# Kernel optimization log

Measured on AMD Instinct MI355X. Metric: run time of the kernel, lower is better.

## Reference

```python
import jax, jax.numpy as jnp
import numpy as np

BN_EPS = 1e-5


def setup_inputs() -> dict:
    key = jax.random.key(0)
    ks = jax.random.split(key, 6)
    B, C, N, K, T, O = 8, 64, 4096, 20, 3, 64
    feat = jax.random.normal(ks[0], (B, C, N), dtype=jnp.float32)
    idx = jax.random.randint(ks[1], (B, N, K), 0, N, dtype=jnp.int32)
    group_pc = jax.random.normal(ks[2], (B, 3, N, K), dtype=jnp.float32)
    weights = jax.random.normal(ks[3], (B, 20, T, N, K), dtype=jnp.float32) * 0.05
    conv_w = jax.random.normal(ks[4], (O, C * T, K), dtype=jnp.float32) * 0.02
    gamma = jnp.ones((O,), dtype=jnp.float32)
    beta = jnp.zeros((O,), dtype=jnp.float32)
    return {"feat": feat, "idx": idx, "group_pc": group_pc, "weights": weights,
            "conv_w": conv_w, "gamma": gamma, "beta": beta}


def _poly_terms(group_pc):
    # group_pc: (B, 3, N, K) -> 20 Taylor terms (B, 20, N, K)
    X, Y, Z = group_pc[:, 0], group_pc[:, 1], group_pc[:, 2]
    XX, YY, ZZ = X * X, Y * Y, Z * Z
    XY, XZ, YZ = X * Y, X * Z, Y * Z
    ones = jnp.ones_like(X)
    return jnp.stack([
        ones, X, Y, Z,
        XX, YY, ZZ,
        XX * X, YY * Y, ZZ * Z,
        XY, XZ, YZ,
        X * XY, X * XZ, Y * YZ, Y * XY, Z * XZ, Z * YZ, XY * Z,
    ], axis=1)


def reference(feat, idx, group_pc, weights, conv_w, gamma, beta):
    B, C, N = feat.shape
    K = idx.shape[-1]
    T = weights.shape[2]
    # KNN gather: group_feat[b, c, n, j] = feat[b, c, idx[b, n, j]]  -> (B, C, N, K)
    group_feat = jax.vmap(lambda f, i: f[:, i])(feat, idx)
    # 20 polynomial basis terms of XYZ: (B, 20, N, K)
    terms = _poly_terms(group_pc)
    # taylor[b, t, n, k] = sum_p weights[b, p, t, n, k] * terms[b, p, n, k]
    taylor = jnp.einsum('bptnk,bpnk->btnk', weights, terms)
    # Fused outer-product + [1, K] conv (output width 1, no bias since bn=True):
    # out[b, o, n] = sum_{c, t, k} group_feat[b,c,n,k] * taylor[b,t,n,k] * W[o, c*T+t, k]
    w = conv_w.reshape(conv_w.shape[0], C, T, K)
    out = jnp.einsum('bcnk,btnk,octk->bon', group_feat, taylor, w)
    # BatchNorm (training-mode batch stats over B and N) + ReLU
    mean = jnp.mean(out, axis=(0, 2), keepdims=True)
    var = jnp.var(out, axis=(0, 2), keepdims=True)
    out = gamma[None, :, None] * (out - mean) / jnp.sqrt(var + BN_EPS) + beta[None, :, None]
    return jax.nn.relu(out)
```

## Files before the change

### kernel.cpp

```cpp
#include <hip/hip_runtime.h>
#include <hip/hip_bf16.h>

#define B_ 8
#define C_ 64
#define N_ 4096
#define K_ 20
#define T_ 3
#define O_ 64
#define P_ 20
#define NK_ (N_ * K_)
#define BN_EPS 1e-5f
#define PADW 68

#define WS_FEATT 0
#define WS_WT (WS_FEATT + B_ * N_ * C_)
#define WS_RAW (WS_WT + 122880)
#define WS_PART (WS_RAW + B_ * O_ * N_)
#define WS_STATS (WS_PART + 512 * O_ * 2)

typedef __attribute__((ext_vector_type(8))) _Float16 half8;
typedef __attribute__((ext_vector_type(2))) _Float16 half2v;
typedef __attribute__((ext_vector_type(2))) __fp16 fp16x2;
typedef __attribute__((ext_vector_type(16))) float f32x16;

union UH8 {
    uint4 u;
    half8 h;
    half2v h2[4];
};
union UH2 {
    unsigned u;
    half2v h;
    fp16x2 f;
};

__device__ inline half2v cvt_pkrtz(float a, float b) {
    UH2 x;
    x.f = __builtin_amdgcn_cvt_pkrtz(a, b);
    return x.h;
}
__device__ inline unsigned cvt_pkrtz_u(float a, float b) {
    UH2 x;
    x.f = __builtin_amdgcn_cvt_pkrtz(a, b);
    return x.u;
}

__global__ void k_transpose_feat(const float* __restrict__ feat, float* __restrict__ featT) {
    __shared__ float t[64][65];
    int bid = blockIdx.x;
    int b = bid & 7;
    int n0 = (bid >> 3) << 6;
    int lx = threadIdx.x & 63, ly = threadIdx.x >> 6;
    const float* fp = feat + b * C_ * N_;
#pragma unroll
    for (int cc = 0; cc < 16; ++cc) {
        int c = ly * 16 + cc;
        t[c][lx] = fp[c * N_ + n0 + lx];
    }
    __syncthreads();
    float* op = featT + (b * N_ + n0) * C_;
#pragma unroll
    for (int u = 0; u < 16; ++u) {
        int n = ly * 16 + u;
        op[n * C_ + lx] = t[lx][n];
    }
}

__global__ void k_pack_w(const float* __restrict__ cw, _Float16* __restrict__ Wh) {
    int e = blockIdx.x * 256 + threadIdx.x;
    int j = e & 7;
    int l = (e >> 3) & 63;
    int frag = e >> 9;
    int oh = frag & 1;
    int cc = (frag >> 1) & 3;
    int kt = frag >> 3;
    int t = kt % 3, k = kt / 3;
    int o = oh * 32 + (l & 31);
    int c = cc * 16 + (l >> 5) * 8 + j;
    Wh[e] = (_Float16)cw[o * (C_ * T_ * K_) + (c * T_ + t) * K_ + k];
}

__global__ __launch_bounds__(512, 4) void k_main(const float* __restrict__ featT,
                                                 const _Float16* __restrict__ Wh,
                                                 const float* __restrict__ weights,
                                                 const float* __restrict__ gpc,
                                                 const int* __restrict__ idx,
                                                 float* __restrict__ raw,
                                                 float* __restrict__ part) {
    __shared__ float G[2][64][PADW];
    __shared__ union {
        struct {
            unsigned tayH[3][K_][64];
            int idxS[K_][64];
        } s;
        float out[64][68];
    } su;

    const int bid0 = blockIdx.x;
    const int bid = (bid0 & 7) * 64 + (bid0 >> 3);
    const int b = bid >> 6;
    const int n0 = (bid & 63) << 6;
    const int tid = threadIdx.x;
    const int lane = tid & 63;
    const int wv = tid >> 6;
    const int wc = wv & 3;
    const int wo = wv >> 2;
    const int nl = lane & 31;
    const int kf = lane >> 5;

    {
        const int* ip = idx + (b * N_ + n0) * K_;
        for (int e = tid; e < 64 * K_; e += 512) su.s.idxS[e % K_][e / K_] = ip[e];
    }
    {
        const float* gpcb = gpc + (size_t)b * 3 * NK_ + n0 * K_;
        const float* wb = weights + (size_t)b * P_ * T_ * NK_ + n0 * K_;
        for (int e = tid; e < 64 * K_; e += 512) {
            float X = gpcb[e];
            float Y = gpcb[NK_ + e];
            float Z = gpcb[2 * NK_ + e];
            float XX = X * X, YY = Y * Y, ZZ = Z * Z;
            float XY = X * Y, XZ = X * Z, YZ = Y * Z;
            float terms[20];
            terms[0] = 1.f; terms[1] = X;      terms[2] = Y;       terms[3] = Z;
            terms[4] = XX;  terms[5] = YY;     terms[6] = ZZ;
            terms[7] = XX * X; terms[8] = YY * Y; terms[9] = ZZ * Z;
            terms[10] = XY; terms[11] = XZ;    terms[12] = YZ;
            terms[13] = X * XY;
            terms[14] = X * XZ;
            terms[15] = Y * YZ;
            terms[16] = Y * XY;
            terms[17] = Z * XZ;
            terms[18] = Z * YZ;
            terms[19] = XY * Z;
            float a0 = 0.f, a1 = 0.f, a2 = 0.f;
            const float* wp = wb + e;
#pragma unroll
            for (int p = 0; p < P_; ++p) {
                float tp = terms[p];
                a0 += wp[0] * tp;
                a1 += wp[NK_] * tp;
                a2 += wp[2 * NK_] * tp;
                wp += 3 * NK_;
            }
            int n = e / K_, k = e - n * K_;
            su.s.tayH[0][k][n] = cvt_pkrtz_u(a0, a0);
            su.s.tayH[1][k][n] = cvt_pkrtz_u(a1, a1);
            su.s.tayH[2][k][n] = cvt_pkrtz_u(a2, a2);
        }
    }
    __syncthreads();

    f32x16 acc[2];
#pragma unroll
    for (int nh = 0; nh < 2; ++nh)
#pragma unroll
        for (int i = 0; i < 16; ++i) acc[nh][i] = 0.f;

    const float* fb = featT + (size_t)b * N_ * C_;
    const int r1 = tid >> 4, r2 = r1 + 32, sseg = tid & 15;

    float4 st1 = *(const float4*)(fb + su.s.idxS[0][r1] * C_ + sseg * 4);
    float4 st2 = *(const float4*)(fb + su.s.idxS[0][r2] * C_ + sseg * 4);

    for (int k = 0; k < K_; ++k) {
        float* Gb = &G[k & 1][0][0];
        *(float4*)(Gb + r1 * PADW + sseg * 4) = st1;
        *(float4*)(Gb + r2 * PADW + sseg * 4) = st2;
        __syncthreads();
        if (k + 1 < K_) {
            st1 = *(const float4*)(fb + su.s.idxS[k + 1][r1] * C_ + sseg * 4);
            st2 = *(const float4*)(fb + su.s.idxS[k + 1][r2] * C_ + sseg * 4);
        }
        const float* row0 = Gb + nl * PADW + wc * 16 + kf * 8;
        const float* row1 = Gb + (nl + 32) * PADW + wc * 16 + kf * 8;
        float4 u0 = *(const float4*)row0, u1 = *(const float4*)(row0 + 4);
        float4 w0 = *(const float4*)row1, w1 = *(const float4*)(row1 + 4);
        half2v h0[4], h1[4];
        h0[0] = cvt_pkrtz(u0.x, u0.y);
        h0[1] = cvt_pkrtz(u0.z, u0.w);
        h0[2] = cvt_pkrtz(u1.x, u1.y);
        h0[3] = cvt_pkrtz(u1.z, u1.w);
        h1[0] = cvt_pkrtz(w0.x, w0.y);
        h1[1] = cvt_pkrtz(w0.z, w0.w);
        h1[2] = cvt_pkrtz(w1.x, w1.y);
        h1[3] = cvt_pkrtz(w1.z, w1.w);
#pragma unroll
        for (int t = 0; t < 3; ++t) {
            UH8 ar;
            ar.u = *(const uint4*)(Wh +
                                   (size_t)((((k * 3 + t) * 4 + wc) * 2 + wo) * 64 + lane) * 8);
            UH2 tv0, tv1;
            tv0.u = su.s.tayH[t][k][nl];
            tv1.u = su.s.tayH[t][k][nl + 32];
            UH8 b0, b1;
#pragma unroll
            for (int i = 0; i < 4; ++i) {
                b0.h2[i] = h0[i] * tv0.h;
                b1.h2[i] = h1[i] * tv1.h;
            }
            acc[0] = __builtin_amdgcn_mfma_f32_32x32x16_f16(ar.h, b0.h, acc[0], 0, 0, 0);
            acc[1] = __builtin_amdgcn_mfma_f32_32x32x16_f16(ar.h, b1.h, acc[1], 0, 0, 0);
        }
    }

    __syncthreads();
#pragma unroll 1
    for (int ww = 0; ww < 4; ++ww) {
        if (wc == ww) {
#pragma unroll
            for (int nh = 0; nh < 2; ++nh)
#pragma unroll
                for (int r = 0; r < 16; ++r) {
                    int row = wo * 32 + (r & 3) + ((r >> 2) << 3) + (kf << 2);
                    int col = nh * 32 + nl;
                    if (ww == 0)
                        su.out[row][col] = acc[nh][r];
                    else
                        su.out[row][col] += acc[nh][r];
                }
        }
        __syncthreads();
    }

    if (tid < 256) {
        int o = tid >> 2, seg = tid & 3;
        float4* dst = (float4*)(raw + ((b * O_ + o) * N_) + n0 + seg * 16);
        const float* srow = &su.out[o][seg * 16];
        dst[0] = *(const float4*)&srow[0];
        dst[1] = *(const float4*)&srow[4];
        dst[2] = *(const float4*)&srow[8];
        dst[3] = *(const float4*)&srow[12];
    }
    if (tid < 64) {
        float s1 = 0.f, s2 = 0.f;
#pragma unroll 8
        for (int n = 0; n < 64; ++n) {
            float v = su.out[tid][n];
            s1 += v;
            s2 += v * v;
        }
        part[(bid * 64 + tid) * 2 + 0] = s1;
        part[(bid * 64 + tid) * 2 + 1] = s2;
    }
}

__global__ void k_bnstats(const float* __restrict__ part, const float* __restrict__ gamma,
                          const float* __restrict__ beta, float* __restrict__ stats) {
    int o = blockIdx.x;
    int tid = threadIdx.x;
    __shared__ float s1s[256], s2s[256];
    float s1 = 0.f, s2 = 0.f;
    for (int j = tid; j < 512; j += 256) {
        s1 += part[(j * 64 + o) * 2 + 0];
        s2 += part[(j * 64 + o) * 2 + 1];
    }
    s1s[tid] = s1;
    s2s[tid] = s2;
    __syncthreads();
    for (int s = 128; s > 0; s >>= 1) {
        if (tid < s) {
            s1s[tid] += s1s[tid + s];
            s2s[tid] += s2s[tid + s];
        }
        __syncthreads();
    }
    if (tid == 0) {
        const float cnt = (float)(B_ * N_);
        float mean = s1s[0] / cnt;
        float var = s2s[0] / cnt - mean * mean;
        float sc = gamma[o] * rsqrtf(var + BN_EPS);
        stats[o * 2 + 0] = sc;
        stats[o * 2 + 1] = beta[o] - mean * sc;
    }
}

__global__ void k_finalize(const float* __restrict__ raw, const float* __restrict__ stats,
                           float* __restrict__ out) {
    int e = (blockIdx.x * 256 + threadIdx.x) * 4;
    int o = (e >> 12) & 63;
    float sc = stats[o * 2 + 0], sh = stats[o * 2 + 1];
    float4 v = *(const float4*)(raw + e);
    v.x = fmaxf(v.x * sc + sh, 0.f);
    v.y = fmaxf(v.y * sc + sh, 0.f);
    v.z = fmaxf(v.z * sc + sh, 0.f);
    v.w = fmaxf(v.w * sc + sh, 0.f);
    *(float4*)(out + e) = v;
}

extern "C" void kernel_launch(void* const* d_in, const int* in_sizes, int n_in,
                              void* d_out, int out_size, void* d_ws, size_t ws_size,
                              hipStream_t stream) {
    const float* feat = (const float*)d_in[0];
    const int* idx = (const int*)d_in[1];
    const float* gpc = (const float*)d_in[2];
    const float* weights = (const float*)d_in[3];
    const float* conv_w = (const float*)d_in[4];
    const float* gamma = (const float*)d_in[5];
    const float* beta = (const float*)d_in[6];
    float* out = (float*)d_out;
    float* ws = (float*)d_ws;

    float* featT = ws + WS_FEATT;
    _Float16* Wh = (_Float16*)(ws + WS_WT);
    float* raw = ws + WS_RAW;
    float* part = ws + WS_PART;
    float* stats = ws + WS_STATS;

    hipLaunchKernelGGL(k_transpose_feat, dim3(512), dim3(256), 0, stream, feat, featT);
    hipLaunchKernelGGL(k_pack_w, dim3((K_ * T_ * C_ * O_) / 256), dim3(256), 0, stream, conv_w,
                       Wh);
    hipLaunchKernelGGL(k_main, dim3(B_ * (N_ / 64)), dim3(512), 0, stream, featT, Wh, weights,
                       gpc, idx, raw, part);
    hipLaunchKernelGGL(k_bnstats, dim3(O_), dim3(256), 0, stream, part, gamma, beta, stats);
    hipLaunchKernelGGL(k_finalize, dim3(B_ * O_ * N_ / 4 / 256), dim3(256), 0, stream, raw, stats,
                       out);
}
```

Before: 74.60 us.

## Split Taylor computation into separate kernel and triple-buffer fp16 gathered features

Moves the per-point Taylor weight contraction (reading the large weights tensor) out of k_main into a dedicated fully-parallel k_taylor kernel that writes fp32 results to workspace, which k_main then loads and converts. The gathered feature tile is now converted to fp16 before being stored in LDS, halving LDS footprint and read traffic. The gather prefetch depth rises from one to three steps with a fully unrolled K loop. The cost is an extra kernel launch and an extra round trip of the Taylor tensor through global memory, plus more registers held for prefetch.

```diff
diff --git a/kernel.cpp b/kernel.cpp
--- a/kernel.cpp
+++ b/kernel.cpp
@@ -10,11 +10,11 @@
 #define P_ 20
 #define NK_ (N_ * K_)
 #define BN_EPS 1e-5f
-#define PADW 68
 
 #define WS_FEATT 0
 #define WS_WT (WS_FEATT + B_ * N_ * C_)
-#define WS_RAW (WS_WT + 122880)
+#define WS_TAY (WS_WT + 122880)
+#define WS_RAW (WS_TAY + B_ * T_ * NK_)
 #define WS_PART (WS_RAW + B_ * O_ * N_)
 #define WS_STATS (WS_PART + 512 * O_ * 2)
 
@@ -34,11 +34,6 @@
     fp16x2 f;
 };
 
-__device__ inline half2v cvt_pkrtz(float a, float b) {
-    UH2 x;
-    x.f = __builtin_amdgcn_cvt_pkrtz(a, b);
-    return x.h;
-}
 __device__ inline unsigned cvt_pkrtz_u(float a, float b) {
     UH2 x;
     x.f = __builtin_amdgcn_cvt_pkrtz(a, b);
@@ -80,17 +75,56 @@
     Wh[e] = (_Float16)cw[o * (C_ * T_ * K_) + (c * T_ + t) * K_ + k];
 }
 
+__global__ void k_taylor(const float* __restrict__ W5, const float* __restrict__ gpc,
+                         float* __restrict__ tay) {
+    int bid0 = blockIdx.x;
+    int bid = (bid0 & 7) * 320 + (bid0 >> 3);
+    int tid = bid * 256 + threadIdx.x;
+    int b = tid / NK_;
+    int nk = tid - b * NK_;
+    const float X = gpc[b * 3 * NK_ + nk];
+    const float Y = gpc[b * 3 * NK_ + NK_ + nk];
+    const float Z = gpc[b * 3 * NK_ + 2 * NK_ + nk];
+    float XX = X * X, YY = Y * Y, ZZ = Z * Z;
+    float XY = X * Y, XZ = X * Z, YZ = Y * Z;
+    float terms[20];
+    terms[0] = 1.f; terms[1] = X;      terms[2] = Y;       terms[3] = Z;
+    terms[4] = XX;  terms[5] = YY;     terms[6] = ZZ;
+    terms[7] = XX * X; terms[8] = YY * Y; terms[9] = ZZ * Z;
+    terms[10] = XY; terms[11] = XZ;    terms[12] = YZ;
+    terms[13] = X * XY;
+    terms[14] = X * XZ;
+    terms[15] = Y * YZ;
+    terms[16] = Y * XY;
+    terms[17] = Z * XZ;
+    terms[18] = Z * YZ;
+    terms[19] = XY * Z;
+    float a0 = 0.f, a1 = 0.f, a2 = 0.f;
+    const float* wp = W5 + (size_t)b * P_ * T_ * NK_ + nk;
+#pragma unroll
+    for (int p = 0; p < P_; ++p) {
+        float tp = terms[p];
+        a0 += wp[0] * tp;
+        a1 += wp[NK_] * tp;
+        a2 += wp[2 * NK_] * tp;
+        wp += 3 * NK_;
+    }
+    float* tp = tay + (size_t)b * T_ * NK_ + nk;
+    tp[0] = a0;
+    tp[NK_] = a1;
+    tp[2 * NK_] = a2;
+}
+
 __global__ __launch_bounds__(512, 4) void k_main(const float* __restrict__ featT,
                                                  const _Float16* __restrict__ Wh,
-                                                 const float* __restrict__ weights,
-                                                 const float* __restrict__ gpc,
+                                                 const float* __restrict__ tay,
                                                  const int* __restrict__ idx,
                                                  float* __restrict__ raw,
                                                  float* __restrict__ part) {
-    __shared__ float G[2][64][PADW];
+    __shared__ unsigned short Gh[3][64][72];
     __shared__ union {
         struct {
-            unsigned tayH[3][K_][64];
+            unsigned tayH[T_][K_][64];
             int idxS[K_][64];
         } s;
         float out[64][68];
@@ -113,40 +147,13 @@
         for (int e = tid; e < 64 * K_; e += 512) su.s.idxS[e % K_][e / K_] = ip[e];
     }
     {
-        const float* gpcb = gpc + (size_t)b * 3 * NK_ + n0 * K_;
-        const float* wb = weights + (size_t)b * P_ * T_ * NK_ + n0 * K_;
-        for (int e = tid; e < 64 * K_; e += 512) {
-            float X = gpcb[e];
-            float Y = gpcb[NK_ + e];
-            float Z = gpcb[2 * NK_ + e];
-            float XX = X * X, YY = Y * Y, ZZ = Z * Z;
-            float XY = X * Y, XZ = X * Z, YZ = Y * Z;
-            float terms[20];
-            terms[0] = 1.f; terms[1] = X;      terms[2] = Y;       terms[3] = Z;
-            terms[4] = XX;  terms[5] = YY;     terms[6] = ZZ;
-            terms[7] = XX * X; terms[8] = YY * Y; terms[9] = ZZ * Z;
-            terms[10] = XY; terms[11] = XZ;    terms[12] = YZ;
-            terms[13] = X * XY;
-            terms[14] = X * XZ;
-            terms[15] = Y * YZ;
-            terms[16] = Y * XY;
-            terms[17] = Z * XZ;
-            terms[18] = Z * YZ;
-            terms[19] = XY * Z;
-            float a0 = 0.f, a1 = 0.f, a2 = 0.f;
-            const float* wp = wb + e;
-#pragma unroll
-            for (int p = 0; p < P_; ++p) {
-                float tp = terms[p];
-                a0 += wp[0] * tp;
-                a1 += wp[NK_] * tp;
-                a2 += wp[2 * NK_] * tp;
-                wp += 3 * NK_;
+#pragma unroll
+        for (int t = 0; t < 3; ++t) {
+            const float* tp = tay + ((size_t)(b * 3 + t) * N_ + n0) * K_;
+            for (int e = tid; e < 64 * K_; e += 512) {
+                float v = tp[e];
+                su.s.tayH[t][e % K_][e / K_] = cvt_pkrtz_u(v, v);
             }
-            int n = e / K_, k = e - n * K_;
-            su.s.tayH[0][k][n] = cvt_pkrtz_u(a0, a0);
-            su.s.tayH[1][k][n] = cvt_pkrtz_u(a1, a1);
-            su.s.tayH[2][k][n] = cvt_pkrtz_u(a2, a2);
         }
     }
     __syncthreads();
@@ -160,31 +167,31 @@
     const float* fb = featT + (size_t)b * N_ * C_;
     const int r1 = tid >> 4, r2 = r1 + 32, sseg = tid & 15;
 
-    float4 st1 = *(const float4*)(fb + su.s.idxS[0][r1] * C_ + sseg * 4);
-    float4 st2 = *(const float4*)(fb + su.s.idxS[0][r2] * C_ + sseg * 4);
-
+    float4 stA[3], stB[3];
+#pragma unroll
+    for (int j = 0; j < 3; ++j) {
+        stA[j] = *(const float4*)(fb + su.s.idxS[j][r1] * C_ + sseg * 4);
+        stB[j] = *(const float4*)(fb + su.s.idxS[j][r2] * C_ + sseg * 4);
+    }
+
+#pragma unroll
     for (int k = 0; k < K_; ++k) {
-        float* Gb = &G[k & 1][0][0];
-        *(float4*)(Gb + r1 * PADW + sseg * 4) = st1;
-        *(float4*)(Gb + r2 * PADW + sseg * 4) = st2;
+        const int buf = k % 3;
+        uint2 wA, wB;
+        wA.x = cvt_pkrtz_u(stA[buf].x, stA[buf].y);
+        wA.y = cvt_pkrtz_u(stA[buf].z, stA[buf].w);
+        wB.x = cvt_pkrtz_u(stB[buf].x, stB[buf].y);
+        wB.y = cvt_pkrtz_u(stB[buf].z, stB[buf].w);
+        *(uint2*)&Gh[buf][r1][sseg * 4] = wA;
+        *(uint2*)&Gh[buf][r2][sseg * 4] = wB;
         __syncthreads();
-        if (k + 1 < K_) {
-            st1 = *(const float4*)(fb + su.s.idxS[k + 1][r1] * C_ + sseg * 4);
-            st2 = *(const float4*)(fb + su.s.idxS[k + 1][r2] * C_ + sseg * 4);
-        }
-        const float* row0 = Gb + nl * PADW + wc * 16 + kf * 8;
-        const float* row1 = Gb + (nl + 32) * PADW + wc * 16 + kf * 8;
-        float4 u0 = *(const float4*)row0, u1 = *(const float4*)(row0 + 4);
-        float4 w0 = *(const float4*)row1, w1 = *(const float4*)(row1 + 4);
-        half2v h0[4], h1[4];
-        h0[0] = cvt_pkrtz(u0.x, u0.y);
-        h0[1] = cvt_pkrtz(u0.z, u0.w);
-        h0[2] = cvt_pkrtz(u1.x, u1.y);
-        h0[3] = cvt_pkrtz(u1.z, u1.w);
-        h1[0] = cvt_pkrtz(w0.x, w0.y);
-        h1[1] = cvt_pkrtz(w0.z, w0.w);
-        h1[2] = cvt_pkrtz(w1.x, w1.y);
-        h1[3] = cvt_pkrtz(w1.z, w1.w);
+        if (k + 3 < K_) {
+            stA[buf] = *(const float4*)(fb + su.s.idxS[k + 3][r1] * C_ + sseg * 4);
+            stB[buf] = *(const float4*)(fb + su.s.idxS[k + 3][r2] * C_ + sseg * 4);
+        }
+        UH8 g0, g1;
+        g0.u = *(const uint4*)&Gh[buf][nl][wc * 16 + kf * 8];
+        g1.u = *(const uint4*)&Gh[buf][nl + 32][wc * 16 + kf * 8];
 #pragma unroll
         for (int t = 0; t < 3; ++t) {
             UH8 ar;
@@ -196,8 +203,8 @@
             UH8 b0, b1;
 #pragma unroll
             for (int i = 0; i < 4; ++i) {
-                b0.h2[i] = h0[i] * tv0.h;
-                b1.h2[i] = h1[i] * tv1.h;
+                b0.h2[i] = g0.h2[i] * tv0.h;
+                b1.h2[i] = g1.h2[i] * tv1.h;
             }
             acc[0] = __builtin_amdgcn_mfma_f32_32x32x16_f16(ar.h, b0.h, acc[0], 0, 0, 0);
             acc[1] = __builtin_amdgcn_mfma_f32_32x32x16_f16(ar.h, b1.h, acc[1], 0, 0, 0);
@@ -303,6 +310,7 @@
 
     float* featT = ws + WS_FEATT;
     _Float16* Wh = (_Float16*)(ws + WS_WT);
+    float* tay = ws + WS_TAY;
     float* raw = ws + WS_RAW;
     float* part = ws + WS_PART;
     float* stats = ws + WS_STATS;
@@ -310,8 +318,9 @@
     hipLaunchKernelGGL(k_transpose_feat, dim3(512), dim3(256), 0, stream, feat, featT);
     hipLaunchKernelGGL(k_pack_w, dim3((K_ * T_ * C_ * O_) / 256), dim3(256), 0, stream, conv_w,
                        Wh);
-    hipLaunchKernelGGL(k_main, dim3(B_ * (N_ / 64)), dim3(512), 0, stream, featT, Wh, weights,
-                       gpc, idx, raw, part);
+    hipLaunchKernelGGL(k_taylor, dim3(B_ * NK_ / 256), dim3(256), 0, stream, weights, gpc, tay);
+    hipLaunchKernelGGL(k_main, dim3(B_ * (N_ / 64)), dim3(512), 0, stream, featT, Wh, tay, idx,
+                       raw, part);
     hipLaunchKernelGGL(k_bnstats, dim3(O_), dim3(256), 0, stream, part, gamma, beta, stats);
     hipLaunchKernelGGL(k_finalize, dim3(B_ * O_ * N_ / 4 / 256), dim3(256), 0, stream, raw, stats,
                        out);
```

New measurement: 80.76 us. 1.08x slower.

## Halve point tile to 32 per block and stage gathered features as fp16

Applied to the files above, without the earlier changes.

The main kernel now handles 32 points per block instead of 64, doubling the grid to 1024 blocks. Each wave keeps one MFMA accumulator instead of two, and the launch bound asks for 8 waves per SIMD. Gathered neighbor features are converted to fp16 before the LDS store, which halves shared-memory traffic and footprint. The aim is more occupancy and more latency hiding for the gather and weight loads. The cost is that each Wh fragment now feeds only one MFMA, so weight reloads double, and the BN partials buffer and reduction double in size.

```diff
diff --git a/kernel.cpp b/kernel.cpp
--- a/kernel.cpp
+++ b/kernel.cpp
@@ -10,13 +10,12 @@
 #define P_ 20
 #define NK_ (N_ * K_)
 #define BN_EPS 1e-5f
-#define PADW 68
 
 #define WS_FEATT 0
 #define WS_WT (WS_FEATT + B_ * N_ * C_)
 #define WS_RAW (WS_WT + 122880)
 #define WS_PART (WS_RAW + B_ * O_ * N_)
-#define WS_STATS (WS_PART + 512 * O_ * 2)
+#define WS_STATS (WS_PART + 131072)
 
 typedef __attribute__((ext_vector_type(8))) _Float16 half8;
 typedef __attribute__((ext_vector_type(2))) _Float16 half2v;
@@ -34,11 +33,6 @@
     fp16x2 f;
 };
 
-__device__ inline half2v cvt_pkrtz(float a, float b) {
-    UH2 x;
-    x.f = __builtin_amdgcn_cvt_pkrtz(a, b);
-    return x.h;
-}
 __device__ inline unsigned cvt_pkrtz_u(float a, float b) {
     UH2 x;
     x.f = __builtin_amdgcn_cvt_pkrtz(a, b);
@@ -80,26 +74,26 @@
     Wh[e] = (_Float16)cw[o * (C_ * T_ * K_) + (c * T_ + t) * K_ + k];
 }
 
-__global__ __launch_bounds__(512, 4) void k_main(const float* __restrict__ featT,
+__global__ __launch_bounds__(512, 8) void k_main(const float* __restrict__ featT,
                                                  const _Float16* __restrict__ Wh,
                                                  const float* __restrict__ weights,
                                                  const float* __restrict__ gpc,
                                                  const int* __restrict__ idx,
                                                  float* __restrict__ raw,
                                                  float* __restrict__ part) {
-    __shared__ float G[2][64][PADW];
+    __shared__ unsigned short Gh[2][32][72];
     __shared__ union {
         struct {
-            unsigned tayH[3][K_][64];
-            int idxS[K_][64];
+            unsigned tayH[T_][K_][32];
+            int idxS[K_][32];
         } s;
-        float out[64][68];
+        float out[64][36];
     } su;
 
     const int bid0 = blockIdx.x;
-    const int bid = (bid0 & 7) * 64 + (bid0 >> 3);
-    const int b = bid >> 6;
-    const int n0 = (bid & 63) << 6;
+    const int bid = (bid0 & 7) * 128 + (bid0 >> 3);
+    const int b = bid >> 7;
+    const int n0 = (bid & 127) << 5;
     const int tid = threadIdx.x;
     const int lane = tid & 63;
     const int wv = tid >> 6;
@@ -110,12 +104,12 @@
 
     {
         const int* ip = idx + (b * N_ + n0) * K_;
-        for (int e = tid; e < 64 * K_; e += 512) su.s.idxS[e % K_][e / K_] = ip[e];
+        for (int e = tid; e < 32 * K_; e += 512) su.s.idxS[e % K_][e / K_] = ip[e];
     }
     {
         const float* gpcb = gpc + (size_t)b * 3 * NK_ + n0 * K_;
-        const float* wb = weights + (size_t)b * P_ * T_ * NK_ + n0 * K_;
-        for (int e = tid; e < 64 * K_; e += 512) {
+        const float* wb0 = weights + (size_t)b * P_ * T_ * NK_ + n0 * K_;
+        for (int e = tid; e < 32 * K_; e += 512) {
             float X = gpcb[e];
             float Y = gpcb[NK_ + e];
             float Z = gpcb[2 * NK_ + e];
@@ -134,16 +128,16 @@
             terms[18] = Z * YZ;
             terms[19] = XY * Z;
             float a0 = 0.f, a1 = 0.f, a2 = 0.f;
-            const float* wp = wb + e;
+            const float* wp = wb0 + e;
 #pragma unroll
             for (int p = 0; p < P_; ++p) {
                 float tp = terms[p];
                 a0 += wp[0] * tp;
-                a1 += wp[NK_] * tp;
-                a2 += wp[2 * NK_] * tp;
-                wp += 3 * NK_;
+                a1 += wp[(size_t)NK_] * tp;
+                a2 += wp[2 * (size_t)NK_] * tp;
+                wp += 3 * (size_t)NK_;
             }
-            int n = e / K_, k = e - n * K_;
+            int n = e / K_, k = e - (e / K_) * K_;
             su.s.tayH[0][k][n] = cvt_pkrtz_u(a0, a0);
             su.s.tayH[1][k][n] = cvt_pkrtz_u(a1, a1);
             su.s.tayH[2][k][n] = cvt_pkrtz_u(a2, a2);
@@ -151,56 +145,38 @@
     }
     __syncthreads();
 
-    f32x16 acc[2];
-#pragma unroll
-    for (int nh = 0; nh < 2; ++nh)
-#pragma unroll
-        for (int i = 0; i < 16; ++i) acc[nh][i] = 0.f;
+    f32x16 acc;
+#pragma unroll
+    for (int i = 0; i < 16; ++i) acc[i] = 0.f;
 
     const float* fb = featT + (size_t)b * N_ * C_;
-    const int r1 = tid >> 4, r2 = r1 + 32, sseg = tid & 15;
-
-    float4 st1 = *(const float4*)(fb + su.s.idxS[0][r1] * C_ + sseg * 4);
-    float4 st2 = *(const float4*)(fb + su.s.idxS[0][r2] * C_ + sseg * 4);
+    const int r = tid >> 4, sseg = tid & 15;
+
+    float4 st = *(const float4*)(fb + su.s.idxS[0][r] * C_ + sseg * 4);
 
     for (int k = 0; k < K_; ++k) {
-        float* Gb = &G[k & 1][0][0];
-        *(float4*)(Gb + r1 * PADW + sseg * 4) = st1;
-        *(float4*)(Gb + r2 * PADW + sseg * 4) = st2;
+        const int buf = k & 1;
+        uint2 w;
+        w.x = cvt_pkrtz_u(st.x, st.y);
+        w.y = cvt_pkrtz_u(st.z, st.w);
+        *(uint2*)&Gh[buf][r][sseg * 4] = w;
         __syncthreads();
         if (k + 1 < K_) {
-            st1 = *(const float4*)(fb + su.s.idxS[k + 1][r1] * C_ + sseg * 4);
-            st2 = *(const float4*)(fb + su.s.idxS[k + 1][r2] * C_ + sseg * 4);
-        }
-        const float* row0 = Gb + nl * PADW + wc * 16 + kf * 8;
-        const float* row1 = Gb + (nl + 32) * PADW + wc * 16 + kf * 8;
-        float4 u0 = *(const float4*)row0, u1 = *(const float4*)(row0 + 4);
-        float4 w0 = *(const float4*)row1, w1 = *(const float4*)(row1 + 4);
-        half2v h0[4], h1[4];
-        h0[0] = cvt_pkrtz(u0.x, u0.y);
-        h0[1] = cvt_pkrtz(u0.z, u0.w);
-        h0[2] = cvt_pkrtz(u1.x, u1.y);
-        h0[3] = cvt_pkrtz(u1.z, u1.w);
-        h1[0] = cvt_pkrtz(w0.x, w0.y);
-        h1[1] = cvt_pkrtz(w0.z, w0.w);
-        h1[2] = cvt_pkrtz(w1.x, w1.y);
-        h1[3] = cvt_pkrtz(w1.z, w1.w);
+            st = *(const float4*)(fb + su.s.idxS[k + 1][r] * C_ + sseg * 4);
+        }
+        UH8 g;
+        g.u = *(const uint4*)&Gh[buf][nl][wc * 16 + kf * 8];
 #pragma unroll
         for (int t = 0; t < 3; ++t) {
             UH8 ar;
             ar.u = *(const uint4*)(Wh +
                                    (size_t)((((k * 3 + t) * 4 + wc) * 2 + wo) * 64 + lane) * 8);
-            UH2 tv0, tv1;
-            tv0.u = su.s.tayH[t][k][nl];
-            tv1.u = su.s.tayH[t][k][nl + 32];
-            UH8 b0, b1;
-#pragma unroll
-            for (int i = 0; i < 4; ++i) {
-                b0.h2[i] = h0[i] * tv0.h;
-                b1.h2[i] = h1[i] * tv1.h;
-            }
-            acc[0] = __builtin_amdgcn_mfma_f32_32x32x16_f16(ar.h, b0.h, acc[0], 0, 0, 0);
-            acc[1] = __builtin_amdgcn_mfma_f32_32x32x16_f16(ar.h, b1.h, acc[1], 0, 0, 0);
+            UH2 tv;
+            tv.u = su.s.tayH[t][k][nl];
+            UH8 bv;
+#pragma unroll
+            for (int i = 0; i < 4; ++i) bv.h2[i] = g.h2[i] * tv.h;
+            acc = __builtin_amdgcn_mfma_f32_32x32x16_f16(ar.h, bv.h, acc, 0, 0, 0);
         }
     }
 
@@ -209,33 +185,27 @@
     for (int ww = 0; ww < 4; ++ww) {
         if (wc == ww) {
 #pragma unroll
-            for (int nh = 0; nh < 2; ++nh)
-#pragma unroll
-                for (int r = 0; r < 16; ++r) {
-                    int row = wo * 32 + (r & 3) + ((r >> 2) << 3) + (kf << 2);
-                    int col = nh * 32 + nl;
-                    if (ww == 0)
-                        su.out[row][col] = acc[nh][r];
-                    else
-                        su.out[row][col] += acc[nh][r];
-                }
+            for (int rr = 0; rr < 16; ++rr) {
+                int row = wo * 32 + (rr & 3) + ((rr >> 2) << 3) + (kf << 2);
+                if (ww == 0)
+                    su.out[row][nl] = acc[rr];
+                else
+                    su.out[row][nl] += acc[rr];
+            }
         }
         __syncthreads();
     }
 
-    if (tid < 256) {
-        int o = tid >> 2, seg = tid & 3;
-        float4* dst = (float4*)(raw + ((b * O_ + o) * N_) + n0 + seg * 16);
-        const float* srow = &su.out[o][seg * 16];
-        dst[0] = *(const float4*)&srow[0];
-        dst[1] = *(const float4*)&srow[4];
-        dst[2] = *(const float4*)&srow[8];
-        dst[3] = *(const float4*)&srow[12];
+    {
+        int o = tid >> 3, seg = tid & 7;
+        float4* dst = (float4*)(raw + ((b * O_ + o) * N_) + n0 + seg * 4);
+        const float* srow = &su.out[o][seg * 4];
+        *dst = make_float4(srow[0], srow[1], srow[2], srow[3]);
     }
     if (tid < 64) {
         float s1 = 0.f, s2 = 0.f;
 #pragma unroll 8
-        for (int n = 0; n < 64; ++n) {
+        for (int n = 0; n < 32; ++n) {
             float v = su.out[tid][n];
             s1 += v;
             s2 += v * v;
@@ -251,7 +221,7 @@
     int tid = threadIdx.x;
     __shared__ float s1s[256], s2s[256];
     float s1 = 0.f, s2 = 0.f;
-    for (int j = tid; j < 512; j += 256) {
+    for (int j = tid; j < 1024; j += 256) {
         s1 += part[(j * 64 + o) * 2 + 0];
         s2 += part[(j * 64 + o) * 2 + 1];
     }
@@ -310,7 +280,7 @@
     hipLaunchKernelGGL(k_transpose_feat, dim3(512), dim3(256), 0, stream, feat, featT);
     hipLaunchKernelGGL(k_pack_w, dim3((K_ * T_ * C_ * O_) / 256), dim3(256), 0, stream, conv_w,
                        Wh);
-    hipLaunchKernelGGL(k_main, dim3(B_ * (N_ / 64)), dim3(512), 0, stream, featT, Wh, weights,
+    hipLaunchKernelGGL(k_main, dim3(B_ * (N_ / 32)), dim3(512), 0, stream, featT, Wh, weights,
                        gpc, idx, raw, part);
     hipLaunchKernelGGL(k_bnstats, dim3(O_), dim3(256), 0, stream, part, gamma, beta, stats);
     hipLaunchKernelGGL(k_finalize, dim3(B_ * O_ * N_ / 4 / 256), dim3(256), 0, stream, raw, stats,
```

New measurement: 78.22 us. 4.9% more time.
